# Performance work log

Hardware: AMD Instinct MI355X
Metric: run time of the kernel (lower is better)

The kernel has to match this reference:

```python
import jax, jax.numpy as jnp
import numpy as np

N = 10000; E = 320000; NFEAT = 500; NHID = 256; C = 16; K = 64
GAMMA = 4; ALPHA = 0.1; BETA = 1.0; EPS = 0.1; LAMDA = 0.5; W1 = 0.5

def _init(key, shape, scale=0.05):
    return jax.random.normal(key, shape, dtype=jnp.float32) * scale

def setup_inputs():
    key = jax.random.key(0)
    ks = jax.random.split(key, 24)
    return {
        "x": jax.random.normal(ks[0], (N, NFEAT), dtype=jnp.float32),
        "edge_index": jax.random.randint(ks[1], (2, E), 0, N),
        "edge_weight": jax.random.uniform(ks[2], (E,), dtype=jnp.float32),
        "adj_weight": jax.random.uniform(ks[3], (E,), dtype=jnp.float32),
        "connect": jax.random.uniform(ks[4], (N, N), dtype=jnp.float32),
        "confidence_in": jax.random.uniform(ks[5], (2, E), dtype=jnp.float32),
        "lin1_w": _init(ks[6], (NHID, NFEAT)),
        "lin1_b": jnp.zeros((NHID,), jnp.float32),
        "lin2_w": _init(ks[7], (C, NHID)),
        "lin2_b": jnp.zeros((C,), jnp.float32),
        "lin_a_w": _init(ks[8], (NHID, N), 0.01),
        "lin_a_b": jnp.zeros((NHID,), jnp.float32),
        "lin_n_w": _init(ks[9], (C, C)),
        "lin_n_b": jnp.zeros((C,), jnp.float32),
        "left_w": _init(ks[10], (C, C)),
        "att_w": _init(ks[11], (1, C)),
        "v_w": _init(ks[12], (K, NHID)),
        "v_b": jnp.zeros((K,), jnp.float32),
        "W": _init(ks[13], (C, C)),
        "conf_param": jnp.zeros((3,), jnp.float32),
        "b_param": jnp.zeros((1,), jnp.float32),
    }

def _forward(x, edge_index, edge_weight, adj_weight, connect, confidence_in,
             lin1_w, lin1_b, lin2_w, lin2_b, lin_a_w, lin_a_b, lin_n_w, lin_n_b,
             left_w, att_w, v_w, v_b, W, conf_param, b_param):
    row, col = edge_index[0], edge_index[1]

    def spmm(vals, out_idx, M):
        # COO sparse @ dense: scatter-add per-edge vals * gathered rows of M
        return jax.ops.segment_sum(vals[:, None] * M, out_idx, num_segments=N)

    x_a = connect @ lin_a_w.T + lin_a_b            # [N, NHID]
    h = x @ lin1_w.T + lin1_b
    h = jax.nn.relu((1.0 - LAMDA) * h + LAMDA * x_a)
    raw = h                                        # [N, NHID]
    h = h @ lin2_w.T + lin2_b                      # [N, C]

    # neighbor label distribution: row-normalized adj @ one_hot(argmax softmax)
    y_hat = jnp.argmax(jax.nn.softmax(h, axis=1), axis=1)
    one_hot = jax.nn.one_hot(y_hat, C, dtype=h.dtype)
    nei = spmm(adj_weight, row, one_hot[col])
    s = nei.sum(axis=1, keepdims=True)
    nei = jnp.where(s != 0, nei / jnp.where(s == 0, 1.0, s), 0.0)

    x_n = jax.nn.relu(nei @ lin_n_w.T + lin_n_b)
    h = (1.0 - W1) * h + W1 * x_n
    init = h

    # per-edge attention-based confidence mixed with input confidences
    lx = h @ left_w.T
    confi = jax.nn.relu(lx[row] + lx[col])
    confi = jax.nn.sigmoid((confi @ att_w.T)[:, 0])
    w = jax.nn.softmax(conf_param)
    conf = confi * w[0] + confidence_in[0] * w[1] + confidence_in[1] * w[2]  # [E]

    V = raw @ v_w.T + v_b                          # [N, K]
    U = spmm(adj_weight, row, V[col]) @ jnp.linalg.inv(V.T @ V)
    eyeK = jnp.eye(K, dtype=h.dtype)

    def edge_mask_score(score):
        S = score ** 2
        ss = jnp.sort(S)
        q1, q3 = ss[E // 4], ss[3 * E // 4]
        thr = (q3 + 1.5 * (q3 - q1)) * conf        # [E]
        mask = (S < thr).astype(h.dtype)
        return (score + b_param[0]) * mask

    def update_u(U, V):
        SS = edge_mask_score(edge_weight - jnp.sum(U[row] * V[col], axis=1))
        temp = spmm(SS, row, V[col]) + U @ (V.T @ V) + EPS * (h @ (h.T @ V))
        inver = jnp.linalg.inv((1.0 + EPS) * (V.T @ V) + BETA * eyeK)
        return temp @ inver

    def update_v(U, V):
        SS = edge_mask_score(edge_weight - jnp.sum(V[row] * U[col], axis=1))
        # A^T @ U: scatter over col with U[row]
        temp = spmm(SS, col, U[row]) + V @ (U.T @ U) + EPS * (h @ (h.T @ U))
        inver = jnp.linalg.inv((1.0 + EPS) * (U.T @ U) + BETA * eyeK)
        return temp @ inver

    for j in range(GAMMA):
        if j % 2 == 0:
            U = update_u(U, V)
        else:
            V = update_v(U, V)

    prop = U @ (h.T @ V).T                         # [N, C]
    out = (1.0 - ALPHA) * prop + ALPHA * init
    return out @ W

def reference(x, edge_index, edge_weight, adj_weight, connect, confidence_in,
              lin1_w, lin1_b, lin2_w, lin2_b, lin_a_w, lin_a_b, lin_n_w, lin_n_b,
              left_w, att_w, v_w, v_b, W, conf_param, b_param):
    return _forward(x, edge_index, edge_weight, adj_weight, connect, confidence_in,
                    lin1_w, lin1_b, lin2_w, lin2_b, lin_a_w, lin_a_b, lin_n_w, lin_n_b,
                    left_w, att_w, v_w, v_b, W, conf_param, b_param)
```

## Files before the change

kernel.cpp:

```cpp
#include <hip/hip_runtime.h>
#include <cstddef>
#include <cstdint>


constexpr int kN  = 10000;
constexpr int kE  = 320000;
constexpr int kNH = 256;
constexpr int kC  = 16;
constexpr int kK  = 64;
constexpr int GRAM_PARTS = 256;
constexpr int PHASE_BLOCKS = 768;

struct SelState {
  int bin1[2]; int rem1[2];
  float thr_base;
};

typedef short bf16x8 __attribute__((ext_vector_type(8)));
typedef float f32x4 __attribute__((ext_vector_type(4)));
typedef ushort ushort8 __attribute__((ext_vector_type(8)));

__device__ __forceinline__ ushort f2bf(float x) {
  unsigned u = __float_as_uint(x);
  unsigned r = (u + 0x7fffu + ((u >> 16) & 1u)) >> 16;
  return (ushort)r;
}
__device__ __forceinline__ float bf2f(ushort h) {
  return __uint_as_float((unsigned)h << 16);
}
__device__ __forceinline__ int swz(int row, int byteInRow) {
  int chunk = (byteInRow >> 4) ^ ((row >> 1) & 3);
  return row * 64 + (chunk << 4) + (byteInRow & 15);
}

__global__ void split_bf(const float* __restrict__ B, ushort* __restrict__ hi,
                         ushort* __restrict__ lo, int N2, int K, int Kp)
{
  int t = blockIdx.x * 256 + threadIdx.x;
  if (t >= N2 * Kp) return;
  int r = t / Kp, c = t % Kp;
  float v = (c < K) ? B[(size_t)r * K + c] : 0.f;
  ushort h = f2bf(v);
  hi[t] = h;
  lo[t] = f2bf(v - bf2f(h));
}

template<int BN, bool ALO>
__global__ __launch_bounds__(256) void gemm_v3(
    const float* __restrict__ A, const ushort* __restrict__ Bhg,
    const ushort* __restrict__ Blg, const float* __restrict__ bias,
    float* __restrict__ out, int M, int K, int Kp, int KR, int outStride)
{
  __shared__ __align__(16) char sAh[64 * 64];
  __shared__ __align__(16) char sAl[ALO ? 64 * 64 : 16];
  __shared__ __align__(16) char sBh[BN * 64];
  __shared__ __align__(16) char sBl[BN * 64];
  const int t = threadIdx.x;
  const int lane = t & 63, w = t >> 6;
  const int bm = blockIdx.x * 64;
  const int k0 = blockIdx.z * KR;
  const int kend = min(K, k0 + KR);
  out += (size_t)blockIdx.z * M * outStride;
  constexpr int WN = BN / 64;
  constexpr int RB = WN;
  const int wc = (w % WN) * 64;
  const int wr = (w / WN) * (RB * 16);
  const int l15 = lane & 15;
  const int lByte = (lane >> 4) * 16;
  const int ar = t >> 2, ac = t & 3;

  f32x4 acc[RB][4] = {};
  for (int kt = k0; kt < kend; kt += 32) {
    {
      int gr = bm + ar, gk = kt + ac * 8;
      float v[8];
      if (gr < M && gk + 8 <= kend) {
        float4 v0 = *reinterpret_cast<const float4*>(A + (size_t)gr * K + gk);
        float4 v1 = *reinterpret_cast<const float4*>(A + (size_t)gr * K + gk + 4);
        v[0] = v0.x; v[1] = v0.y; v[2] = v0.z; v[3] = v0.w;
        v[4] = v1.x; v[5] = v1.y; v[6] = v1.z; v[7] = v1.w;
      } else {
#pragma unroll
        for (int q = 0; q < 8; q++)
          v[q] = (gr < M && gk + q < kend) ? A[(size_t)gr * K + gk + q] : 0.f;
      }
      ushort8 h8, l8;
#pragma unroll
      for (int q = 0; q < 8; q++) {
        ushort h = f2bf(v[q]); h8[q] = h;
        if (ALO) l8[q] = f2bf(v[q] - bf2f(h));
      }
      *reinterpret_cast<ushort8*>(sAh + swz(ar, ac * 16)) = h8;
      if (ALO) *reinterpret_cast<ushort8*>(sAl + swz(ar, ac * 16)) = l8;
    }
#pragma unroll
    for (int i2 = 0; i2 < BN / 64; i2++) {
      int idx = t + i2 * 256;
      int r = idx >> 2, c = idx & 3;
      size_t gb = (size_t)r * Kp + kt + c * 8;
      ushort8 hv = *reinterpret_cast<const ushort8*>(Bhg + gb);
      ushort8 lv = *reinterpret_cast<const ushort8*>(Blg + gb);
      *reinterpret_cast<ushort8*>(sBh + swz(r, c * 16)) = hv;
      *reinterpret_cast<ushort8*>(sBl + swz(r, c * 16)) = lv;
    }
    __syncthreads();
    bf16x8 bh[4], bl[4];
#pragma unroll
    for (int nbq = 0; nbq < 4; nbq++) {
      int rr = wc + nbq * 16 + l15;
      bh[nbq] = *reinterpret_cast<const bf16x8*>(sBh + swz(rr, lByte));
      bl[nbq] = *reinterpret_cast<const bf16x8*>(sBl + swz(rr, lByte));
    }
#pragma unroll
    for (int rb = 0; rb < RB; rb++) {
      int rr = wr + rb * 16 + l15;
      bf16x8 ah = *reinterpret_cast<const bf16x8*>(sAh + swz(rr, lByte));
#pragma unroll
      for (int nbq = 0; nbq < 4; nbq++) {
        acc[rb][nbq] = __builtin_amdgcn_mfma_f32_16x16x32_bf16(ah, bh[nbq], acc[rb][nbq], 0, 0, 0);
        acc[rb][nbq] = __builtin_amdgcn_mfma_f32_16x16x32_bf16(ah, bl[nbq], acc[rb][nbq], 0, 0, 0);
      }
      if (ALO) {
        bf16x8 al = *reinterpret_cast<const bf16x8*>(sAl + swz(rr, lByte));
#pragma unroll
        for (int nbq = 0; nbq < 4; nbq++)
          acc[rb][nbq] = __builtin_amdgcn_mfma_f32_16x16x32_bf16(al, bh[nbq], acc[rb][nbq], 0, 0, 0);
      }
    }
    __syncthreads();
  }
#pragma unroll
  for (int rb = 0; rb < RB; rb++) {
#pragma unroll
    for (int nbq = 0; nbq < 4; nbq++) {
      int colg = wc + nbq * 16 + l15;
      float bv = bias ? bias[colg] : 0.f;
#pragma unroll
      for (int jj = 0; jj < 4; jj++) {
        int rowg = bm + wr + rb * 16 + (lane >> 4) * 4 + jj;
        if (rowg < M) out[(size_t)rowg * outStride + colg] = acc[rb][nbq][jj] + bv;
      }
    }
  }
}

__global__ void reduce_raw(const float4* __restrict__ Pa, const float4* px,
                           const float* __restrict__ ba, const float* __restrict__ b1,
                           float4* rawOut, int* cntR, int* cntC, int* fillR,
                           int* fillC, float* nei)
{
  int t = blockIdx.x * 256 + threadIdx.x;
  if (t < kN) { cntR[t] = 0; cntC[t] = 0; fillR[t] = 0; fillC[t] = 0; }
  if (t < kN * kC) nei[t] = 0.f;
  if (t >= kN * kNH / 4) return;
  const int sl = kN * kNH / 4;
  float4 s = Pa[t];
#pragma unroll
  for (int p = 1; p < 6; p++) {
    float4 q = Pa[t + (size_t)p * sl];
    s.x += q.x; s.y += q.y; s.z += q.z; s.w += q.w;
  }
  float4 pxv = px[t];
  int c4 = t & 63;
  float4 vba = reinterpret_cast<const float4*>(ba)[c4];
  float4 vb1 = reinterpret_cast<const float4*>(b1)[c4];
  float4 r;
  r.x = fmaxf(0.5f * (s.x + vba.x) + 0.5f * (pxv.x + vb1.x), 0.f);
  r.y = fmaxf(0.5f * (s.y + vba.y) + 0.5f * (pxv.y + vb1.y), 0.f);
  r.z = fmaxf(0.5f * (s.z + vba.z) + 0.5f * (pxv.z + vb1.z), 0.f);
  r.w = fmaxf(0.5f * (s.w + vba.w) + 0.5f * (pxv.w + vb1.w), 0.f);
  rawOut[t] = r;
}

struct MegaArgs {
  const float* raw;
  const float* lin2_w; const float* lin2_b;
  const int* row; const int* col;
  const float* aw; const float* ew;
  const float* lnw; const float* lnb;
  const float* left_w; const float* att_w;
  const float* ci; const float* conf_p; const float* b_param;
  const float* Wm;
  float* h16; int* yhat; float* nei; float* hC; float* lx; float* conf;
  int* cntR; int* cntC; int* fillR; int* fillC; int* startR; int* startC;
  int* eR; int* eC; int* othR; int* othC;
  float* Va; float* Vb; float* Ua; float* Ub; float* T;
  float* score; float* G; float* Gi; float* Gp; float* hTX; float* Hp;
  int* hist1; int* h2a; int* h2b;
  float* P;
  SelState* sel;
  float* out;
};

__device__ __forceinline__ void uv_at(const MegaArgs& a, int j,
                                      float*& Ucur, float*& Unxt,
                                      float*& Vcur, float*& Vnxt)
{
  int uU = (j >= 1) + (j >= 3);
  int uV = (j >= 2) + (j >= 4);
  Ucur = (uU & 1) ? a.Ub : a.Ua; Unxt = (uU & 1) ? a.Ua : a.Ub;
  Vcur = (uV & 1) ? a.Vb : a.Va; Vnxt = (uV & 1) ? a.Va : a.Vb;
}

__device__ void gram2_dev(const float* M, const float* hc, float* P, int b, float* shm)
{
  float* sM = shm;
  float* sH = shm + 512;
  const int t = threadIdx.x;
  const int aG = t >> 2, cG0 = (t & 3) * 16;
  const int aH = t >> 4, cH0 = (t & 15) * 4;
  float accG[16]; float accH[4];
#pragma unroll
  for (int q = 0; q < 16; q++) accG[q] = 0.f;
#pragma unroll
  for (int q = 0; q < 4; q++) accH[q] = 0.f;
  int r0 = b * 40, r1 = min(kN, r0 + 40);
  for (int rb = r0; rb < r1; rb += 8) {
    int nb2 = min(8, r1 - rb);
    __syncthreads();
    for (int q = t; q < nb2 * 64; q += 256) sM[q] = M[(size_t)rb * 64 + q];
    for (int q = t; q < nb2 * 16; q += 256) sH[q] = hc[(size_t)rb * 16 + q];
    __syncthreads();
    for (int r = 0; r < nb2; r++) {
      float avG = sM[r * 64 + aG];
      const float* sbG = &sM[r * 64 + cG0];
#pragma unroll
      for (int q = 0; q < 16; q++) accG[q] += avG * sbG[q];
      float avH = sH[r * 16 + aH];
      const float* sbH = &sM[r * 64 + cH0];
#pragma unroll
      for (int q = 0; q < 4; q++) accH[q] += avH * sbH[q];
    }
  }
  float* p1 = P + (size_t)b * 5120 + aG * 64 + cG0;
#pragma unroll
  for (int q = 0; q < 16; q++) p1[q] = accG[q];
  float* p2 = P + (size_t)b * 5120 + 4096 + aH * 64 + cH0;
#pragma unroll
  for (int q = 0; q < 4; q++) p2[q] = accH[q];
}

__device__ void inverse_dev(const float* G, float* Gi, float alpha, float beta,
                            const float* hTX, float* Gp, float* Hp, float* shm)
{
  float* A = shm;
  float* prow = shm + 8448;
  float* fcol = shm + 8576;
  const int t = threadIdx.x;
  for (int q = t; q < 64 * 128; q += 256) {
    int r = q >> 7, c = q & 127;
    float v;
    if (c < 64) v = alpha * G[r * 64 + c] + ((c == r) ? beta : 0.f);
    else        v = (c - 64 == r) ? 1.f : 0.f;
    A[r * 132 + c] = v;
  }
  __syncthreads();
  const int i  = t >> 2;
  const int c0 = (t & 3) * 32;
  for (int k = 0; k < 64; k++) {
    if (t < 128) prow[t] = A[k * 132 + t];
    else if (t < 192) fcol[t - 128] = A[(t - 128) * 132 + k];
    __syncthreads();
    float pinv = 1.f / prow[k];
    float f = fcol[i];
    float4* Ar = reinterpret_cast<float4*>(&A[i * 132 + c0]);
    const float4* pr = reinterpret_cast<const float4*>(&prow[c0]);
    if (i == k) {
#pragma unroll
      for (int q = 0; q < 8; q++) {
        float4 p = pr[q];
        p.x *= pinv; p.y *= pinv; p.z *= pinv; p.w *= pinv;
        Ar[q] = p;
      }
    } else {
#pragma unroll
      for (int q = 0; q < 8; q++) {
        float4 p = pr[q]; float4 av = Ar[q];
        av.x -= f * (p.x * pinv); av.y -= f * (p.y * pinv);
        av.z -= f * (p.z * pinv); av.w -= f * (p.w * pinv);
        Ar[q] = av;
      }
    }
    __syncthreads();
  }
  for (int q = t; q < 4096; q += 256) Gi[q] = A[(q >> 6) * 132 + 64 + (q & 63)];
  if (Gp) {
    for (int q = t; q < 4096; q += 256) {
      int r = q >> 6, k = q & 63;
      float s = 0.f;
#pragma unroll 8
      for (int jj = 0; jj < 64; jj++) s += G[r * 64 + jj] * A[jj * 132 + 64 + k];
      Gp[q] = s;
    }
    for (int q = t; q < 1024; q += 256) {
      int c = q >> 6, k = q & 63;
      float s = 0.f;
#pragma unroll 8
      for (int jj = 0; jj < 64; jj++) s += hTX[c * 64 + jj] * A[jj * 132 + 64 + k];
      Hp[q] = 0.1f * s;
    }
  }
}

__device__ void scan_dev(const int* h0, const int* h1, int stage, SelState* sel, int* shm)
{
  const int t = threadIdx.x;
  int* part = shm;
  int* fbs  = shm + 256;
  float* qsh = (float*)(shm + 258);
  for (int tgt = 0; tgt < 2; tgt++) {
    const int* H = tgt ? h1 : h0;
    const int4* H4 = reinterpret_cast<const int4*>(H + t * 256);
    int R = (stage == 1) ? (tgt ? (3 * kE / 4) : (kE / 4)) : sel->rem1[tgt];
    int lsum = 0;
    for (int b = 0; b < 64; b++) { int4 v = H4[b]; lsum += v.x + v.y + v.z + v.w; }
    part[t] = lsum;
    __syncthreads();
    for (int off = 1; off < 256; off <<= 1) {
      int v = part[t];
      int u = (t >= off) ? part[t - off] : 0;
      __syncthreads();
      part[t] = v + u;
      __syncthreads();
    }
    int cum = part[t] - lsum;
    int fb = -1, fr = 0;
    for (int b = 0; b < 64; b++) {
      int4 v = H4[b];
      int bb = t * 256 + b * 4;
      if (fb < 0 && R >= cum && R < cum + v.x) { fb = bb;     fr = R - cum; } cum += v.x;
      if (fb < 0 && R >= cum && R < cum + v.y) { fb = bb + 1; fr = R - cum; } cum += v.y;
      if (fb < 0 && R >= cum && R < cum + v.z) { fb = bb + 2; fr = R - cum; } cum += v.z;
      if (fb < 0 && R >= cum && R < cum + v.w) { fb = bb + 3; fr = R - cum; } cum += v.w;
    }
    if (fb >= 0) {
      fbs[tgt] = fb;
      if (stage == 1) { sel->bin1[tgt] = fb; sel->rem1[tgt] = fr; }
    }
    __syncthreads();
    if (stage == 2 && t == 0) {
      unsigned u = ((unsigned)sel->bin1[tgt] << 16) | (unsigned)fbs[tgt];
      qsh[tgt] = __uint_as_float(u);
    }
    __syncthreads();
  }
  if (stage == 2 && t == 0) {
    float q1 = qsh[0], q3 = qsh[1];
    sel->thr_base = q3 + 1.5f * (q3 - q1);
  }
}

__device__ void spmm_dev(const float* vals, const float* score, const float* conf,
                         const SelState* sel, const float* bp,
                         const int* start, const int* eids, const int* oth,
                         const float* Msrc, float* T, int wid0, int wstride)
{
  int lane = threadIdx.x & 63;
  float tb = 0.f, bp0 = 0.f;
  if (!vals) { tb = sel->thr_base; bp0 = bp[0]; }
  for (int wid = wid0; wid < kN; wid += wstride) {
    int p = start[wid], pend = start[wid + 1];
    float acc = 0.f;
    for (; p + 4 <= pend; p += 4) {
      int e0 = eids[p], e1 = eids[p + 1], e2 = eids[p + 2], e3 = eids[p + 3];
      int o0 = oth[p], o1 = oth[p + 1], o2 = oth[p + 2], o3 = oth[p + 3];
      float m0 = Msrc[(size_t)o0 * 64 + lane];
      float m1 = Msrc[(size_t)o1 * 64 + lane];
      float m2 = Msrc[(size_t)o2 * 64 + lane];
      float m3 = Msrc[(size_t)o3 * 64 + lane];
      float v0, v1, v2, v3;
      if (vals) { v0 = vals[e0]; v1 = vals[e1]; v2 = vals[e2]; v3 = vals[e3]; }
      else {
        float s0 = score[e0], s1 = score[e1], s2 = score[e2], s3 = score[e3];
        v0 = (s0 * s0 < tb * conf[e0]) ? (s0 + bp0) : 0.f;
        v1 = (s1 * s1 < tb * conf[e1]) ? (s1 + bp0) : 0.f;
        v2 = (s2 * s2 < tb * conf[e2]) ? (s2 + bp0) : 0.f;
        v3 = (s3 * s3 < tb * conf[e3]) ? (s3 + bp0) : 0.f;
      }
      acc += v0 * m0 + v1 * m1 + v2 * m2 + v3 * m3;
    }
    for (; p < pend; ++p) {
      int e = eids[p];
      float v;
      if (vals) v = vals[e];
      else { float sc = score[e]; v = (sc * sc < tb * conf[e]) ? (sc + bp0) : 0.f; }
      acc += v * Msrc[(size_t)oth[p] * 64 + lane];
    }
    T[(size_t)wid * 64 + lane] = acc;
  }
}

__device__ void outf_dev(const MegaArgs& a, const float* T, const float* X,
                         float* Out, int gtid, int gsz)
{
  for (int i = gtid; i < 65536; i += gsz) { a.hist1[i] = 0; a.h2a[i] = 0; a.h2b[i] = 0; }
  for (int t = gtid; t < kN * 16; t += gsz) {
    int i = t >> 4, kq = t & 15;
    const float* ti = T + (size_t)i * 64;
    const float4* G4 = reinterpret_cast<const float4*>(a.Gi);
    float4 s = make_float4(0.f, 0.f, 0.f, 0.f);
#pragma unroll 8
    for (int jj = 0; jj < 64; jj++) {
      float tv = ti[jj];
      float4 g = G4[jj * 16 + kq];
      s.x += tv * g.x; s.y += tv * g.y; s.z += tv * g.z; s.w += tv * g.w;
    }
    if (X) {
      const float* xi = X + (size_t)i * 64;
      const float4* Gp4 = reinterpret_cast<const float4*>(a.Gp);
      float4 s2 = make_float4(0.f, 0.f, 0.f, 0.f);
#pragma unroll 8
      for (int jj = 0; jj < 64; jj++) {
        float xv = xi[jj];
        float4 g = Gp4[jj * 16 + kq];
        s2.x += xv * g.x; s2.y += xv * g.y; s2.z += xv * g.z; s2.w += xv * g.w;
      }
      s.x += s2.x; s.y += s2.y; s.z += s2.z; s.w += s2.w;
      const float4* Hp4 = reinterpret_cast<const float4*>(a.Hp);
      float4 s3 = make_float4(0.f, 0.f, 0.f, 0.f);
#pragma unroll
      for (int c = 0; c < 16; c++) {
        float hv = a.hC[(size_t)i * 16 + c];
        float4 g = Hp4[c * 16 + kq];
        s3.x += hv * g.x; s3.y += hv * g.y; s3.z += hv * g.z; s3.w += hv * g.w;
      }
      s.x += s3.x; s.y += s3.y; s.z += s3.z; s.w += s3.w;
    }
    *reinterpret_cast<float4*>(Out + (size_t)i * 64 + kq * 4) = s;
  }
}

__device__ void reduce_dev(const MegaArgs& a, int gtid, int gsz)
{
  for (int c = gtid; c < 5120; c += gsz) {
    float s = 0.f;
    for (int p = 0; p < GRAM_PARTS; p++) s += a.P[(size_t)p * 5120 + c];
    if (c < 4096) a.G[c] = s;
    else a.hTX[c - 4096] = s;
  }
}

__global__ __launch_bounds__(256, 4) void mega_phase(MegaArgs a, int phase, int j)
{
  __shared__ __align__(16) float smem[8704];
  const int tid = threadIdx.x;
  const int bid = blockIdx.x;
  const int nb  = gridDim.x;
  const int gtid = bid * 256 + tid;
  const int gsz = nb * 256;
  float *Ucur, *Unxt, *Vcur, *Vnxt;
  uv_at(a, j, Ucur, Unxt, Vcur, Vnxt);
  bool up = ((j & 1) == 0);
  const float* Ma   = up ? Ucur : Vcur;
  const float* Mb   = up ? Vcur : Ucur;
  const float* Moth = up ? Vcur : Ucur;
  const float* Xcur = up ? Ucur : Vcur;
  float* Xout       = up ? Unxt : Vnxt;

  switch (phase) {
  case 0: {
    for (int t = gtid; t < kN * 16; t += gsz) {
      int i = t >> 4, jj = t & 15;
      const float4* av4 = reinterpret_cast<const float4*>(a.raw + (size_t)i * 256);
      const float4* bv4 = reinterpret_cast<const float4*>(a.lin2_w + (size_t)jj * 256);
      float s = a.lin2_b[jj];
#pragma unroll 8
      for (int q = 0; q < 64; q++) {
        float4 av = av4[q], bv = bv4[q];
        s += av.x * bv.x + av.y * bv.y + av.z * bv.z + av.w * bv.w;
      }
      a.h16[t] = s;
      float m = s; int am = jj;
#pragma unroll
      for (int off = 1; off < 16; off <<= 1) {
        float om = __shfl_xor(m, off);
        int oa = __shfl_xor(am, off);
        if (om > m || (om == m && oa < am)) { m = om; am = oa; }
      }
      if (jj == 0) a.yhat[i] = am;
    }
  } break;
  case 1: {
    for (int e = gtid; e < kE; e += gsz) {
      int r = a.row[e], c = a.col[e];
      atomicAdd(&a.cntR[r], 1);
      atomicAdd(&a.cntC[c], 1);
      atomicAdd(&a.nei[(size_t)r * 16 + a.yhat[c]], a.aw[e]);
    }
    for (int part = bid; part < GRAM_PARTS; part += nb)
      gram2_dev(a.Va, a.Va , a.P, part, smem);
  } break;
  case 2: {
    if (bid == 0) {
      int* part = (int*)smem;
      for (int pass = 0; pass < 2; ++pass) {
        const int* cnt = pass ? a.cntC : a.cntR;
        int* start = pass ? a.startC : a.startR;
        int bbase = tid * 40;
        int s = 0;
        for (int q = 0; q < 40; q++) { int idx = bbase + q; if (idx < kN) s += cnt[idx]; }
        part[tid] = s;
        __syncthreads();
        for (int off = 1; off < 256; off <<= 1) {
          int v = part[tid];
          int u = (tid >= off) ? part[tid - off] : 0;
          __syncthreads();
          part[tid] = v + u;
          __syncthreads();
        }
        int run = part[tid] - s;
        for (int q = 0; q < 40; q++) {
          int idx = bbase + q;
          if (idx < kN) { start[idx] = run; run += cnt[idx]; }
        }
        if (tid == 255) start[kN] = part[255];
        __syncthreads();
      }
    } else {
      int g2 = (bid - 1) * 256 + tid, s2 = (nb - 1) * 256;
      for (int i = g2; i < kN; i += s2) {
        float nv[16]; float s = 0.f;
#pragma unroll
        for (int c = 0; c < 16; c++) { nv[c] = a.nei[(size_t)i * 16 + c]; s += nv[c]; }
        float inv = (s != 0.f) ? 1.f / s : 0.f;
#pragma unroll
        for (int jj = 0; jj < 16; jj++) {
          float xn = a.lnb[jj];
#pragma unroll
          for (int c = 0; c < 16; c++) xn += (nv[c] * inv) * a.lnw[jj * 16 + c];
          xn = fmaxf(xn, 0.f);
          a.hC[(size_t)i * 16 + jj] = 0.5f * a.h16[(size_t)i * 16 + jj] + 0.5f * xn;
        }
      }
      for (int c = g2; c < 5120; c += s2) {
        float s = 0.f;
        for (int p = 0; p < GRAM_PARTS; p++) s += a.P[(size_t)p * 5120 + c];
        if (c < 4096) a.G[c] = s;
        else a.hTX[c - 4096] = s;
      }
    }
  } break;
  case 3: {
    if (bid == 0) {
      inverse_dev(a.G, a.Gi, 1.0f, 0.0f, nullptr, nullptr, nullptr, smem);
    } else {
      int g2 = (bid - 1) * 256 + tid, s2 = (nb - 1) * 256;
      for (int e = g2; e < kE; e += s2) {
        int r = a.row[e], c = a.col[e];
        int pr = a.startR[r] + atomicAdd(&a.fillR[r], 1);
        a.eR[pr] = e; a.othR[pr] = c;
        int pc = a.startC[c] + atomicAdd(&a.fillC[c], 1);
        a.eC[pc] = e; a.othC[pc] = r;
      }
      for (int t = g2; t < kN * 16; t += s2) {
        int i = t >> 4, jj = t & 15;
        float s = 0.f;
#pragma unroll
        for (int c = 0; c < 16; c++) s += a.hC[(size_t)i * 16 + c] * a.left_w[jj * 16 + c];
        a.lx[t] = s;
      }
    }
  } break;
  case 4: {
    for (int e = gtid; e < kE; e += gsz) {
      float p0 = a.conf_p[0], p1 = a.conf_p[1], p2 = a.conf_p[2];
      float m = fmaxf(p0, fmaxf(p1, p2));
      float e0 = expf(p0 - m), e1 = expf(p1 - m), e2 = expf(p2 - m);
      float inv = 1.f / (e0 + e1 + e2);
      float w0 = e0 * inv, w1 = e1 * inv, w2 = e2 * inv;
      const float* aa = a.lx + (size_t)a.row[e] * 16;
      const float* bb = a.lx + (size_t)a.col[e] * 16;
      float s = 0.f;
#pragma unroll
      for (int c = 0; c < 16; c++) s += fmaxf(aa[c] + bb[c], 0.f) * a.att_w[c];
      float cf = 1.f / (1.f + expf(-s));
      a.conf[e] = cf * w0 + a.ci[e] * w1 + a.ci[(size_t)kE + e] * w2;
    }
    spmm_dev(a.aw, nullptr, nullptr, nullptr, nullptr,
             a.startR, a.eR, a.othR, a.Va, a.T, bid * 4 + (tid >> 6), nb * 4);
  } break;
  case 5: outf_dev(a, a.T, nullptr, a.Ua, gtid, gsz); break;
  case 6: {
    for (int e = gtid; e < kE; e += gsz) {
      const float4* av4 = reinterpret_cast<const float4*>(Ma + (size_t)a.row[e] * 64);
      const float4* bv4 = reinterpret_cast<const float4*>(Mb + (size_t)a.col[e] * 64);
      float s = 0.f;
#pragma unroll
      for (int q = 0; q < 16; q++) {
        float4 av = av4[q], bv = bv4[q];
        s += av.x * bv.x + av.y * bv.y + av.z * bv.z + av.w * bv.w;
      }
      float sc = a.ew[e] - s;
      a.score[e] = sc;
      unsigned u = __float_as_uint(sc * sc);
      atomicAdd(&a.hist1[u >> 16], 1);
    }
  } break;
  case 7: {
    if (bid == 0) scan_dev(a.hist1, a.hist1, 1, a.sel, (int*)smem);
    else for (int part = bid - 1; part < GRAM_PARTS; part += nb - 1)
      gram2_dev(Moth, a.hC, a.P, part, smem);
  } break;
  case 8: {
    reduce_dev(a, gtid, gsz);
    for (int e = gtid; e < kE; e += gsz) {
      float sc = a.score[e];
      unsigned u = __float_as_uint(sc * sc);
      int top = (int)(u >> 16);
      if (top == a.sel->bin1[0]) atomicAdd(&a.h2a[u & 0xFFFF], 1);
      if (top == a.sel->bin1[1]) atomicAdd(&a.h2b[u & 0xFFFF], 1);
    }
  } break;
  case 9: {
    if (bid == 0) scan_dev(a.h2a, a.h2b, 2, a.sel, (int*)smem);
    else if (bid == 1) inverse_dev(a.G, a.Gi, 1.1f, 1.0f, a.hTX, a.Gp, a.Hp, smem);
  } break;
  case 10: {
    if (up) spmm_dev(nullptr, a.score, a.conf, a.sel, a.b_param,
                     a.startR, a.eR, a.othR, Vcur, a.T, bid * 4 + (tid >> 6), nb * 4);
    else    spmm_dev(nullptr, a.score, a.conf, a.sel, a.b_param,
                     a.startC, a.eC, a.othC, Ucur, a.T, bid * 4 + (tid >> 6), nb * 4);
  } break;
  case 11: outf_dev(a, a.T, Xcur, Xout, gtid, gsz); break;
  case 12: {
    for (int part = bid; part < GRAM_PARTS; part += nb)
      gram2_dev(Vcur, a.hC, a.P, part, smem);
  } break;
  case 13: reduce_dev(a, gtid, gsz); break;
  case 14: {
    float* sh = smem;
    float* sW = smem + 1024;
    for (int q = tid; q < 1024; q += 256) sh[q] = a.hTX[q];
    sW[tid] = a.Wm[tid & 255];
    __syncthreads();
    for (int i = gtid; i < kN; i += gsz) {
      const float* u = Ucur + (size_t)i * 64;
      float pre[16];
#pragma unroll
      for (int c = 0; c < 16; c++) {
        float s = 0.f;
#pragma unroll
        for (int k = 0; k < 64; k++) s += u[k] * sh[c * 64 + k];
        pre[c] = 0.9f * s + 0.1f * a.hC[(size_t)i * 16 + c];
      }
#pragma unroll
      for (int jj = 0; jj < 16; jj++) {
        float o = 0.f;
#pragma unroll
        for (int c = 0; c < 16; c++) o += pre[c] * sW[c * 16 + jj];
        a.out[(size_t)i * 16 + jj] = o;
      }
    }
  } break;
  }
}

extern "C" void kernel_launch(void* const* d_in, const int* in_sizes, int n_in,
                              void* d_out, int out_size, void* d_ws, size_t ws_size,
                              hipStream_t stream)
{
  const float* x       = (const float*)d_in[0];
  const int*   eidx    = (const int*)d_in[1];
  const float* ew      = (const float*)d_in[2];
  const float* aw      = (const float*)d_in[3];
  const float* connect = (const float*)d_in[4];
  const float* ci      = (const float*)d_in[5];
  const float* lin1_w  = (const float*)d_in[6];
  const float* lin1_b  = (const float*)d_in[7];
  const float* lin2_w  = (const float*)d_in[8];
  const float* lin2_b  = (const float*)d_in[9];
  const float* lin_a_w = (const float*)d_in[10];
  const float* lin_a_b = (const float*)d_in[11];
  const float* lin_n_w = (const float*)d_in[12];
  const float* lin_n_b = (const float*)d_in[13];
  const float* left_w  = (const float*)d_in[14];
  const float* att_w   = (const float*)d_in[15];
  const float* v_w     = (const float*)d_in[16];
  const float* v_b     = (const float*)d_in[17];
  const float* Wm      = (const float*)d_in[18];
  const float* conf_p  = (const float*)d_in[19];
  const float* b_param = (const float*)d_in[20];
  const int* row = eidx;
  const int* col = eidx + kE;
  float* out = (float*)d_out;

  char* base = (char*)d_ws;
  size_t off = 0;
  auto alloc = [&](size_t bytes) -> void* {
    void* p = base + off;
    off += bytes;
    off = (off + 255) & ~(size_t)255;
    return p;
  };
  float* raw   = (float*)alloc((size_t)kN * kNH * 4);
  float* h16   = (float*)alloc((size_t)kN * kC * 4);
  float* hC    = (float*)alloc((size_t)kN * kC * 4);
  float* nei   = (float*)alloc((size_t)kN * kC * 4);
  float* lx    = (float*)alloc((size_t)kN * kC * 4);
  int*   yhat  = (int*)alloc((size_t)kN * 4);
  float* conf  = (float*)alloc((size_t)kE * 4);
  float* Va    = (float*)alloc((size_t)kN * kK * 4);
  float* Vb    = (float*)alloc((size_t)kN * kK * 4);
  float* Ua    = (float*)alloc((size_t)kN * kK * 4);
  float* Ub    = (float*)alloc((size_t)kN * kK * 4);
  float* T     = (float*)alloc((size_t)kN * kK * 4);
  float* score = (float*)alloc((size_t)kE * 4);
  float* G     = (float*)alloc(64 * 64 * 4);
  float* Gi    = (float*)alloc(64 * 64 * 4);
  float* Gp    = (float*)alloc(64 * 64 * 4);
  float* hTX   = (float*)alloc(kC * kK * 4);
  float* Hp    = (float*)alloc(kC * kK * 4);
  int* hist1   = (int*)alloc(65536 * 4);
  int* h2a     = (int*)alloc(65536 * 4);
  int* h2b     = (int*)alloc(65536 * 4);
  SelState* sel = (SelState*)alloc(sizeof(SelState));
  int* cntR    = (int*)alloc((size_t)kN * 4);
  int* cntC    = (int*)alloc((size_t)kN * 4);
  int* fillR   = (int*)alloc((size_t)kN * 4);
  int* fillC   = (int*)alloc((size_t)kN * 4);
  int* startR  = (int*)alloc((size_t)(kN + 1) * 4);
  int* startC  = (int*)alloc((size_t)(kN + 1) * 4);
  int* eR      = (int*)alloc((size_t)kE * 4);
  int* eC      = (int*)alloc((size_t)kE * 4);
  int* othR    = (int*)alloc((size_t)kE * 4);
  int* othC    = (int*)alloc((size_t)kE * 4);
  float* P     = (float*)alloc((size_t)GRAM_PARTS * 5120 * 4);
  const int KpC = 10016, KpX = 512, KpV = 256;
  ushort* BcH = (ushort*)alloc((size_t)256 * KpC * 2);
  ushort* BcL = (ushort*)alloc((size_t)256 * KpC * 2);
  ushort* BxH = (ushort*)alloc((size_t)256 * KpX * 2);
  ushort* BxL = (ushort*)alloc((size_t)256 * KpX * 2);
  ushort* BvH = (ushort*)alloc((size_t)64 * KpV * 2);
  ushort* BvL = (ushort*)alloc((size_t)64 * KpV * 2);
  float* Pbig  = (float*)alloc((size_t)6 * kN * kNH * 4);

  split_bf<<<(256 * KpC + 255) / 256, 256, 0, stream>>>(lin_a_w, BcH, BcL, 256, 10000, KpC);
  split_bf<<<(256 * KpX + 255) / 256, 256, 0, stream>>>(lin1_w, BxH, BxL, 256, 500, KpX);
  split_bf<<<(64 * KpV + 255) / 256, 256, 0, stream>>>(v_w, BvH, BvL, 64, 256, KpV);

  gemm_v3<256, false><<<dim3(157, 1, 6), 256, 0, stream>>>(
      connect, BcH, BcL, nullptr, Pbig, kN, 10000, KpC, 1696, kNH);
  gemm_v3<256, true><<<dim3(157, 1, 1), 256, 0, stream>>>(
      x, BxH, BxL, nullptr, raw, kN, 500, KpX, 512, kNH);
  reduce_raw<<<(kN * kNH / 4 + 255) / 256, 256, 0, stream>>>(
      (const float4*)Pbig, (const float4*)raw, lin_a_b, lin1_b, (float4*)raw,
      cntR, cntC, fillR, fillC, nei);
  gemm_v3<64, true><<<dim3(157, 1, 1), 256, 0, stream>>>(
      raw, BvH, BvL, v_b, Va, kN, 256, KpV, 256, kK);

  MegaArgs ma;
  ma.raw = raw; ma.lin2_w = lin2_w; ma.lin2_b = lin2_b;
  ma.row = row; ma.col = col; ma.aw = aw; ma.ew = ew;
  ma.lnw = lin_n_w; ma.lnb = lin_n_b; ma.left_w = left_w; ma.att_w = att_w;
  ma.ci = ci; ma.conf_p = conf_p; ma.b_param = b_param; ma.Wm = Wm;
  ma.h16 = h16; ma.yhat = yhat; ma.nei = nei; ma.hC = hC; ma.lx = lx; ma.conf = conf;
  ma.cntR = cntR; ma.cntC = cntC; ma.fillR = fillR; ma.fillC = fillC;
  ma.startR = startR; ma.startC = startC;
  ma.eR = eR; ma.eC = eC; ma.othR = othR; ma.othC = othC;
  ma.Va = Va; ma.Vb = Vb; ma.Ua = Ua; ma.Ub = Ub; ma.T = T;
  ma.score = score; ma.G = G; ma.Gi = Gi; ma.Gp = Gp; ma.hTX = hTX; ma.Hp = Hp;
  ma.hist1 = hist1; ma.h2a = h2a; ma.h2b = h2b;
  ma.P = P; ma.sel = sel; ma.out = out;

  const dim3 pg(PHASE_BLOCKS);
  for (int p = 0; p <= 5; p++) mega_phase<<<pg, 256, 0, stream>>>(ma, p, 0);
  for (int j = 0; j < 4; j++)
    for (int p = 6; p <= 11; p++) mega_phase<<<pg, 256, 0, stream>>>(ma, p, j);
  mega_phase<<<pg, 256, 0, stream>>>(ma, 12, 4);
  mega_phase<<<pg, 256, 0, stream>>>(ma, 13, 4);
  mega_phase<<<pg, 256, 0, stream>>>(ma, 14, 4);
}
```

Measured before the change: 2.084 ms.

## Prefetch GEMM tiles into registers, merge weight splits, and fuse iteration phases

The bf16 split GEMM now loads the next K-tile of A and B into registers while MFMAs run on the current shared-memory tile, hiding global load latency. The three weight-splitting kernels are merged into one launch. In the iterative U/V loop, the histogram scans are computed redundantly by every block so that scan, gram, reduce, inverse and masked SpMM fit into fewer phases, cutting launches per iteration from 6 to 4. The costs are extra registers in the GEMM and duplicated scan work in every block.

```diff
diff --git a/kernel.cpp b/kernel.cpp
--- a/kernel.cpp
+++ b/kernel.cpp
@@ -13,7 +13,6 @@
 
 struct SelState {
   int bin1[2]; int rem1[2];
-  float thr_base;
 };
 
 typedef short bf16x8 __attribute__((ext_vector_type(8)));
@@ -33,16 +32,26 @@
   return row * 64 + (chunk << 4) + (byteInRow & 15);
 }
 
-__global__ void split_bf(const float* __restrict__ B, ushort* __restrict__ hi,
-                         ushort* __restrict__ lo, int N2, int K, int Kp)
-{
+__global__ void split3_bf(const float* __restrict__ Wa, ushort* ha, ushort* la,
+                          const float* __restrict__ Wx, ushort* hx, ushort* lx2,
+                          const float* __restrict__ Wv, ushort* hv, ushort* lv)
+{
+  const int n1 = 256 * 10016, n2 = 256 * 512, n3 = 64 * 256;
   int t = blockIdx.x * 256 + threadIdx.x;
-  if (t >= N2 * Kp) return;
-  int r = t / Kp, c = t % Kp;
-  float v = (c < K) ? B[(size_t)r * K + c] : 0.f;
-  ushort h = f2bf(v);
-  hi[t] = h;
-  lo[t] = f2bf(v - bf2f(h));
+  if (t < n1) {
+    int r = t / 10016, c = t % 10016;
+    float v = (c < 10000) ? Wa[(size_t)r * 10000 + c] : 0.f;
+    ushort h = f2bf(v); ha[t] = h; la[t] = f2bf(v - bf2f(h));
+  } else if (t < n1 + n2) {
+    int q = t - n1;
+    int r = q / 512, c = q % 512;
+    float v = (c < 500) ? Wx[(size_t)r * 500 + c] : 0.f;
+    ushort h = f2bf(v); hx[q] = h; lx2[q] = f2bf(v - bf2f(h));
+  } else if (t < n1 + n2 + n3) {
+    int q = t - n1 - n2;
+    float v = Wv[q];
+    ushort h = f2bf(v); hv[q] = h; lv[q] = f2bf(v - bf2f(h));
+  }
 }
 
 template<int BN, bool ALO>
@@ -69,41 +78,73 @@
   const int lByte = (lane >> 4) * 16;
   const int ar = t >> 2, ac = t & 3;
 
+  float pv[8];
+  ushort8 pbh[WN], pbl[WN];
+
+  {
+    int gr = bm + ar, gk = k0 + ac * 8;
+    if (gr < M && gk + 8 <= kend) {
+      float4 v0 = *reinterpret_cast<const float4*>(A + (size_t)gr * K + gk);
+      float4 v1 = *reinterpret_cast<const float4*>(A + (size_t)gr * K + gk + 4);
+      pv[0] = v0.x; pv[1] = v0.y; pv[2] = v0.z; pv[3] = v0.w;
+      pv[4] = v1.x; pv[5] = v1.y; pv[6] = v1.z; pv[7] = v1.w;
+    } else {
+#pragma unroll
+      for (int q = 0; q < 8; q++)
+        pv[q] = (gr < M && gk + q < kend) ? A[(size_t)gr * K + gk + q] : 0.f;
+    }
+#pragma unroll
+    for (int i2 = 0; i2 < WN; i2++) {
+      int idx = t + i2 * 256;
+      int r = idx >> 2, c = idx & 3;
+      size_t gb = (size_t)r * Kp + k0 + c * 8;
+      pbh[i2] = *reinterpret_cast<const ushort8*>(Bhg + gb);
+      pbl[i2] = *reinterpret_cast<const ushort8*>(Blg + gb);
+    }
+  }
+
   f32x4 acc[RB][4] = {};
   for (int kt = k0; kt < kend; kt += 32) {
     {
-      int gr = bm + ar, gk = kt + ac * 8;
-      float v[8];
+      ushort8 h8, l8;
+#pragma unroll
+      for (int q = 0; q < 8; q++) {
+        ushort h = f2bf(pv[q]); h8[q] = h;
+        if (ALO) l8[q] = f2bf(pv[q] - bf2f(h));
+      }
+      *reinterpret_cast<ushort8*>(sAh + swz(ar, ac * 16)) = h8;
+      if (ALO) *reinterpret_cast<ushort8*>(sAl + swz(ar, ac * 16)) = l8;
+#pragma unroll
+      for (int i2 = 0; i2 < WN; i2++) {
+        int idx = t + i2 * 256;
+        int r = idx >> 2, c = idx & 3;
+        *reinterpret_cast<ushort8*>(sBh + swz(r, c * 16)) = pbh[i2];
+        *reinterpret_cast<ushort8*>(sBl + swz(r, c * 16)) = pbl[i2];
+      }
+    }
+    __syncthreads();
+    int kn = kt + 32;
+    if (kn < kend) {
+      int gr = bm + ar, gk = kn + ac * 8;
       if (gr < M && gk + 8 <= kend) {
         float4 v0 = *reinterpret_cast<const float4*>(A + (size_t)gr * K + gk);
         float4 v1 = *reinterpret_cast<const float4*>(A + (size_t)gr * K + gk + 4);
-        v[0] = v0.x; v[1] = v0.y; v[2] = v0.z; v[3] = v0.w;
-        v[4] = v1.x; v[5] = v1.y; v[6] = v1.z; v[7] = v1.w;
+        pv[0] = v0.x; pv[1] = v0.y; pv[2] = v0.z; pv[3] = v0.w;
+        pv[4] = v1.x; pv[5] = v1.y; pv[6] = v1.z; pv[7] = v1.w;
       } else {
 #pragma unroll
         for (int q = 0; q < 8; q++)
-          v[q] = (gr < M && gk + q < kend) ? A[(size_t)gr * K + gk + q] : 0.f;
-      }
-      ushort8 h8, l8;
-#pragma unroll
-      for (int q = 0; q < 8; q++) {
-        ushort h = f2bf(v[q]); h8[q] = h;
-        if (ALO) l8[q] = f2bf(v[q] - bf2f(h));
-      }
-      *reinterpret_cast<ushort8*>(sAh + swz(ar, ac * 16)) = h8;
-      if (ALO) *reinterpret_cast<ushort8*>(sAl + swz(ar, ac * 16)) = l8;
-    }
-#pragma unroll
-    for (int i2 = 0; i2 < BN / 64; i2++) {
-      int idx = t + i2 * 256;
-      int r = idx >> 2, c = idx & 3;
-      size_t gb = (size_t)r * Kp + kt + c * 8;
-      ushort8 hv = *reinterpret_cast<const ushort8*>(Bhg + gb);
-      ushort8 lv = *reinterpret_cast<const ushort8*>(Blg + gb);
-      *reinterpret_cast<ushort8*>(sBh + swz(r, c * 16)) = hv;
-      *reinterpret_cast<ushort8*>(sBl + swz(r, c * 16)) = lv;
-    }
-    __syncthreads();
+          pv[q] = (gr < M && gk + q < kend) ? A[(size_t)gr * K + gk + q] : 0.f;
+      }
+#pragma unroll
+      for (int i2 = 0; i2 < WN; i2++) {
+        int idx = t + i2 * 256;
+        int r = idx >> 2, c = idx & 3;
+        size_t gb = (size_t)r * Kp + kn + c * 8;
+        pbh[i2] = *reinterpret_cast<const ushort8*>(Bhg + gb);
+        pbl[i2] = *reinterpret_cast<const ushort8*>(Blg + gb);
+      }
+    }
     bf16x8 bh[4], bl[4];
 #pragma unroll
     for (int nbq = 0; nbq < 4; nbq++) {
@@ -302,62 +343,42 @@
   }
 }
 
-__device__ void scan_dev(const int* h0, const int* h1, int stage, SelState* sel, int* shm)
+__device__ void scan_core(const int* H, int R, int* shm, int outSlot)
 {
   const int t = threadIdx.x;
   int* part = shm;
-  int* fbs  = shm + 256;
-  float* qsh = (float*)(shm + 258);
-  for (int tgt = 0; tgt < 2; tgt++) {
-    const int* H = tgt ? h1 : h0;
-    const int4* H4 = reinterpret_cast<const int4*>(H + t * 256);
-    int R = (stage == 1) ? (tgt ? (3 * kE / 4) : (kE / 4)) : sel->rem1[tgt];
-    int lsum = 0;
-    for (int b = 0; b < 64; b++) { int4 v = H4[b]; lsum += v.x + v.y + v.z + v.w; }
-    part[t] = lsum;
+  const int4* H4 = reinterpret_cast<const int4*>(H + t * 256);
+  int lsum = 0;
+  for (int b = 0; b < 64; b++) { int4 v = H4[b]; lsum += v.x + v.y + v.z + v.w; }
+  part[t] = lsum;
+  __syncthreads();
+  for (int off = 1; off < 256; off <<= 1) {
+    int v = part[t];
+    int u = (t >= off) ? part[t - off] : 0;
     __syncthreads();
-    for (int off = 1; off < 256; off <<= 1) {
-      int v = part[t];
-      int u = (t >= off) ? part[t - off] : 0;
-      __syncthreads();
-      part[t] = v + u;
-      __syncthreads();
-    }
-    int cum = part[t] - lsum;
-    int fb = -1, fr = 0;
-    for (int b = 0; b < 64; b++) {
-      int4 v = H4[b];
-      int bb = t * 256 + b * 4;
-      if (fb < 0 && R >= cum && R < cum + v.x) { fb = bb;     fr = R - cum; } cum += v.x;
-      if (fb < 0 && R >= cum && R < cum + v.y) { fb = bb + 1; fr = R - cum; } cum += v.y;
-      if (fb < 0 && R >= cum && R < cum + v.z) { fb = bb + 2; fr = R - cum; } cum += v.z;
-      if (fb < 0 && R >= cum && R < cum + v.w) { fb = bb + 3; fr = R - cum; } cum += v.w;
-    }
-    if (fb >= 0) {
-      fbs[tgt] = fb;
-      if (stage == 1) { sel->bin1[tgt] = fb; sel->rem1[tgt] = fr; }
-    }
+    part[t] = v + u;
     __syncthreads();
-    if (stage == 2 && t == 0) {
-      unsigned u = ((unsigned)sel->bin1[tgt] << 16) | (unsigned)fbs[tgt];
-      qsh[tgt] = __uint_as_float(u);
-    }
-    __syncthreads();
-  }
-  if (stage == 2 && t == 0) {
-    float q1 = qsh[0], q3 = qsh[1];
-    sel->thr_base = q3 + 1.5f * (q3 - q1);
-  }
+  }
+  int cum = part[t] - lsum;
+  int fb = -1, fr = 0;
+  for (int b = 0; b < 64; b++) {
+    int4 v = H4[b];
+    int bb = t * 256 + b * 4;
+    if (fb < 0 && R >= cum && R < cum + v.x) { fb = bb;     fr = R - cum; } cum += v.x;
+    if (fb < 0 && R >= cum && R < cum + v.y) { fb = bb + 1; fr = R - cum; } cum += v.y;
+    if (fb < 0 && R >= cum && R < cum + v.z) { fb = bb + 2; fr = R - cum; } cum += v.z;
+    if (fb < 0 && R >= cum && R < cum + v.w) { fb = bb + 3; fr = R - cum; } cum += v.w;
+  }
+  if (fb >= 0) { shm[outSlot] = fb; shm[outSlot + 1] = fr; }
+  __syncthreads();
 }
 
 __device__ void spmm_dev(const float* vals, const float* score, const float* conf,
-                         const SelState* sel, const float* bp,
+                         float thr, float bp0,
                          const int* start, const int* eids, const int* oth,
                          const float* Msrc, float* T, int wid0, int wstride)
 {
   int lane = threadIdx.x & 63;
-  float tb = 0.f, bp0 = 0.f;
-  if (!vals) { tb = sel->thr_base; bp0 = bp[0]; }
   for (int wid = wid0; wid < kN; wid += wstride) {
     int p = start[wid], pend = start[wid + 1];
     float acc = 0.f;
@@ -372,10 +393,10 @@
       if (vals) { v0 = vals[e0]; v1 = vals[e1]; v2 = vals[e2]; v3 = vals[e3]; }
       else {
         float s0 = score[e0], s1 = score[e1], s2 = score[e2], s3 = score[e3];
-        v0 = (s0 * s0 < tb * conf[e0]) ? (s0 + bp0) : 0.f;
-        v1 = (s1 * s1 < tb * conf[e1]) ? (s1 + bp0) : 0.f;
-        v2 = (s2 * s2 < tb * conf[e2]) ? (s2 + bp0) : 0.f;
-        v3 = (s3 * s3 < tb * conf[e3]) ? (s3 + bp0) : 0.f;
+        v0 = (s0 * s0 < thr * conf[e0]) ? (s0 + bp0) : 0.f;
+        v1 = (s1 * s1 < thr * conf[e1]) ? (s1 + bp0) : 0.f;
+        v2 = (s2 * s2 < thr * conf[e2]) ? (s2 + bp0) : 0.f;
+        v3 = (s3 * s3 < thr * conf[e3]) ? (s3 + bp0) : 0.f;
       }
       acc += v0 * m0 + v1 * m1 + v2 * m2 + v3 * m3;
     }
@@ -383,7 +404,7 @@
       int e = eids[p];
       float v;
       if (vals) v = vals[e];
-      else { float sc = score[e]; v = (sc * sc < tb * conf[e]) ? (sc + bp0) : 0.f; }
+      else { float sc = score[e]; v = (sc * sc < thr * conf[e]) ? (sc + bp0) : 0.f; }
       acc += v * Msrc[(size_t)oth[p] * 64 + lane];
     }
     T[(size_t)wid * 64 + lane] = acc;
@@ -488,7 +509,7 @@
       atomicAdd(&a.nei[(size_t)r * 16 + a.yhat[c]], a.aw[e]);
     }
     for (int part = bid; part < GRAM_PARTS; part += nb)
-      gram2_dev(a.Va, a.Va , a.P, part, smem);
+      gram2_dev(a.Va, a.Va, a.P, part, smem);
   } break;
   case 2: {
     if (bid == 0) {
@@ -576,7 +597,7 @@
       float cf = 1.f / (1.f + expf(-s));
       a.conf[e] = cf * w0 + a.ci[e] * w1 + a.ci[(size_t)kE + e] * w2;
     }
-    spmm_dev(a.aw, nullptr, nullptr, nullptr, nullptr,
+    spmm_dev(a.aw, nullptr, nullptr, 0.f, 0.f,
              a.startR, a.eR, a.othR, a.Va, a.T, bid * 4 + (tid >> 6), nb * 4);
   } break;
   case 5: outf_dev(a, a.T, nullptr, a.Ua, gtid, gsz); break;
@@ -595,39 +616,56 @@
       unsigned u = __float_as_uint(sc * sc);
       atomicAdd(&a.hist1[u >> 16], 1);
     }
+    for (int part = bid; part < GRAM_PARTS; part += nb)
+      gram2_dev(Moth, a.hC, a.P, part, smem);
   } break;
   case 7: {
-    if (bid == 0) scan_dev(a.hist1, a.hist1, 1, a.sel, (int*)smem);
-    else for (int part = bid - 1; part < GRAM_PARTS; part += nb - 1)
-      gram2_dev(Moth, a.hC, a.P, part, smem);
-  } break;
-  case 8: {
     reduce_dev(a, gtid, gsz);
+    int* ishm = (int*)smem;
+    scan_core(a.hist1, kE / 4, ishm, 256);
+    int b0 = ishm[256];
+    if (bid == 0 && tid == 0) { a.sel->bin1[0] = ishm[256]; a.sel->rem1[0] = ishm[257]; }
+    scan_core(a.hist1, 3 * kE / 4, ishm, 258);
+    int b1 = ishm[258];
+    if (bid == 0 && tid == 0) { a.sel->bin1[1] = ishm[258]; a.sel->rem1[1] = ishm[259]; }
     for (int e = gtid; e < kE; e += gsz) {
       float sc = a.score[e];
       unsigned u = __float_as_uint(sc * sc);
       int top = (int)(u >> 16);
-      if (top == a.sel->bin1[0]) atomicAdd(&a.h2a[u & 0xFFFF], 1);
-      if (top == a.sel->bin1[1]) atomicAdd(&a.h2b[u & 0xFFFF], 1);
-    }
-  } break;
-  case 9: {
-    if (bid == 0) scan_dev(a.h2a, a.h2b, 2, a.sel, (int*)smem);
-    else if (bid == 1) inverse_dev(a.G, a.Gi, 1.1f, 1.0f, a.hTX, a.Gp, a.Hp, smem);
-  } break;
+      if (top == b0) atomicAdd(&a.h2a[u & 0xFFFF], 1);
+      if (top == b1) atomicAdd(&a.h2b[u & 0xFFFF], 1);
+    }
+  } break;
+  case 8: {
+    if (bid == 0) {
+      inverse_dev(a.G, a.Gi, 1.1f, 1.0f, a.hTX, a.Gp, a.Hp, smem);
+    } else {
+      int* ishm = (int*)smem;
+      int bA = a.sel->bin1[0], bB = a.sel->bin1[1];
+      int rA = a.sel->rem1[0], rB = a.sel->rem1[1];
+      scan_core(a.h2a, rA, ishm, 256);
+      int f0 = ishm[256];
+      scan_core(a.h2b, rB, ishm, 258);
+      int f1 = ishm[258];
+      float q1 = __uint_as_float(((unsigned)bA << 16) | (unsigned)f0);
+      float q3 = __uint_as_float(((unsigned)bB << 16) | (unsigned)f1);
+      float thr = q3 + 1.5f * (q3 - q1);
+      float bp0 = a.b_param[0];
+      if (up) spmm_dev(nullptr, a.score, a.conf, thr, bp0,
+                       a.startR, a.eR, a.othR, Vcur, a.T,
+                       (bid - 1) * 4 + (tid >> 6), (nb - 1) * 4);
+      else    spmm_dev(nullptr, a.score, a.conf, thr, bp0,
+                       a.startC, a.eC, a.othC, Ucur, a.T,
+                       (bid - 1) * 4 + (tid >> 6), (nb - 1) * 4);
+    }
+  } break;
+  case 9: outf_dev(a, a.T, Xcur, Xout, gtid, gsz); break;
   case 10: {
-    if (up) spmm_dev(nullptr, a.score, a.conf, a.sel, a.b_param,
-                     a.startR, a.eR, a.othR, Vcur, a.T, bid * 4 + (tid >> 6), nb * 4);
-    else    spmm_dev(nullptr, a.score, a.conf, a.sel, a.b_param,
-                     a.startC, a.eC, a.othC, Ucur, a.T, bid * 4 + (tid >> 6), nb * 4);
-  } break;
-  case 11: outf_dev(a, a.T, Xcur, Xout, gtid, gsz); break;
-  case 12: {
     for (int part = bid; part < GRAM_PARTS; part += nb)
       gram2_dev(Vcur, a.hC, a.P, part, smem);
   } break;
-  case 13: reduce_dev(a, gtid, gsz); break;
-  case 14: {
+  case 11: reduce_dev(a, gtid, gsz); break;
+  case 12: {
     float* sh = smem;
     float* sW = smem + 1024;
     for (int q = tid; q < 1024; q += 256) sh[q] = a.hTX[q];
@@ -734,9 +772,11 @@
   ushort* BvL = (ushort*)alloc((size_t)64 * KpV * 2);
   float* Pbig  = (float*)alloc((size_t)6 * kN * kNH * 4);
 
-  split_bf<<<(256 * KpC + 255) / 256, 256, 0, stream>>>(lin_a_w, BcH, BcL, 256, 10000, KpC);
-  split_bf<<<(256 * KpX + 255) / 256, 256, 0, stream>>>(lin1_w, BxH, BxL, 256, 500, KpX);
-  split_bf<<<(64 * KpV + 255) / 256, 256, 0, stream>>>(v_w, BvH, BvL, 64, 256, KpV);
+  {
+    int total = 256 * KpC + 256 * KpX + 64 * KpV;
+    split3_bf<<<(total + 255) / 256, 256, 0, stream>>>(
+        lin_a_w, BcH, BcL, lin1_w, BxH, BxL, v_w, BvH, BvL);
+  }
 
   gemm_v3<256, false><<<dim3(157, 1, 6), 256, 0, stream>>>(
       connect, BcH, BcL, nullptr, Pbig, kN, 10000, KpC, 1696, kNH);
@@ -765,8 +805,8 @@
   const dim3 pg(PHASE_BLOCKS);
   for (int p = 0; p <= 5; p++) mega_phase<<<pg, 256, 0, stream>>>(ma, p, 0);
   for (int j = 0; j < 4; j++)
-    for (int p = 6; p <= 11; p++) mega_phase<<<pg, 256, 0, stream>>>(ma, p, j);
+    for (int p = 6; p <= 9; p++) mega_phase<<<pg, 256, 0, stream>>>(ma, p, j);
+  mega_phase<<<pg, 256, 0, stream>>>(ma, 10, 4);
+  mega_phase<<<pg, 256, 0, stream>>>(ma, 11, 4);
   mega_phase<<<pg, 256, 0, stream>>>(ma, 12, 4);
-  mega_phase<<<pg, 256, 0, stream>>>(ma, 13, 4);
-  mega_phase<<<pg, 256, 0, stream>>>(ma, 14, 4);
-}
+}
```

After: 2.490 ms. 19.5% more time.
